# Kernel optimization log

Hardware: AMD Instinct MI355X
Metric: run time of the kernel (lower is better)

## Reference

```python
import jax, jax.numpy as jnp
import numpy as np
from jax import lax

B, N, D = 8, 1024, 768      # batch, tokens, feature dim
H, Y = 12, 64               # heads, head dim
M = 3072                    # hopfield memories (4*D)
STEPS = 12                  # descent steps (module default)
ALPHA = 0.1                 # SGD step size (module default)
BETA = 1.0 / np.sqrt(Y)     # attention inverse temperature
EPS = 1e-5


def setup_inputs() -> dict:
    key = jax.random.key(0)
    k0, k1, k2, k3 = jax.random.split(key, 4)
    return {
        "x": jax.random.normal(k0, (B, N, D), dtype=jnp.float32),
        "ln_gamma": jnp.ones((D,), dtype=jnp.float32),
        "ln_beta": jnp.zeros((D,), dtype=jnp.float32),
        "wq": jax.random.normal(k1, (H, Y, D), dtype=jnp.float32) * 0.02,
        "wk": jax.random.normal(k2, (H, Y, D), dtype=jnp.float32) * 0.02,
        "xi": jax.random.normal(k3, (M, D), dtype=jnp.float32) * 0.02,
    }


def _layer_norm(x, gamma, beta):
    mu = jnp.mean(x, axis=-1, keepdims=True)
    var = jnp.var(x, axis=-1, keepdims=True)
    return gamma * (x - mu) * lax.rsqrt(var + EPS) + beta


def _energy(g, wq, wk, xi):
    # Attention energy: A[b,h,m,n] = sum_y K_{hy m} Q_{hy n}
    q = jnp.einsum("hyd,bnd->bhny", wq, g)
    k = jnp.einsum("hyd,bnd->bhny", wk, g)
    logits = BETA * jnp.einsum("bhmy,bhny->bhmn", k, q)  # [B,H,N(keys),N(queries)]
    e_att = -(1.0 / BETA) * jnp.sum(jax.scipy.special.logsumexp(logits, axis=2))
    # Hopfield energy: -0.5 * sum relu(xi @ g)^2
    hid = jnp.einsum("md,bnd->bnm", xi, g)
    e_hn = -0.5 * jnp.sum(jnp.square(jax.nn.relu(hid)))
    return e_att + e_hn


_energy_grad = jax.grad(_energy)


def reference(x, ln_gamma, ln_beta, wq, wk, xi):
    def step(x, _):
        g = _layer_norm(x, ln_gamma, ln_beta)  # grad taken w.r.t. g, not through LN
        grad = _energy_grad(g, wq, wk, xi)
        return x - ALPHA * grad, None

    x, _ = lax.scan(step, x, None, length=STEPS)
    return x
```

## Files before the change

kernel.cpp:

```cpp
#include <hip/hip_runtime.h>
#include <math.h>

#define B_ 8
#define N_ 1024
#define D_ 768
#define H_ 12
#define Y_ 64
#define M_ 3072
#define STEPS_ 12
#define ALPHA_ 0.1f
#define BETA_ 0.125f
#define EPS_ 1e-5f

typedef __attribute__((ext_vector_type(8))) short bf16x8;
typedef __attribute__((ext_vector_type(8))) unsigned short u16x8;
typedef __attribute__((ext_vector_type(4))) float f32x4;

__device__ inline unsigned short f2bf(float f) {
  union { float f; unsigned int u; } v; v.f = f;
  unsigned int r = (v.u + 0x7fffu + ((v.u >> 16) & 1u)) >> 16;
  return (unsigned short)r;
}

__device__ inline void async_copy16(const void* g, void* l) {
  __builtin_amdgcn_global_load_lds(
      (const __attribute__((address_space(1))) unsigned int*)g,
      (__attribute__((address_space(3))) unsigned int*)l, 16, 0, 0);
}

__device__ inline int xcd_remap(int bid, int nwg) {
  const int qd = nwg >> 3, rm = nwg & 7;
  const int xcd = bid & 7, idx = bid >> 3;
  return (xcd < rm ? xcd * (qd + 1) : rm * (qd + 1) + (xcd - rm) * qd) + idx;
}

__global__ __launch_bounds__(256) void ln_kernel(const float* __restrict__ x,
    const float* __restrict__ gamma, const float* __restrict__ beta,
    unsigned short* __restrict__ g) {
  const int row = blockIdx.x;
  const int t = threadIdx.x;
  const float* xr = x + (size_t)row * D_;
  float v0 = xr[t], v1 = xr[t + 256], v2 = xr[t + 512];
  float s = v0 + v1 + v2;
  float sq = v0 * v0 + v1 * v1 + v2 * v2;
  #pragma unroll
  for (int off = 1; off < 64; off <<= 1) {
    s += __shfl_xor(s, off);
    sq += __shfl_xor(sq, off);
  }
  __shared__ float ss[4], ssq[4];
  const int wid = t >> 6;
  if ((t & 63) == 0) { ss[wid] = s; ssq[wid] = sq; }
  __syncthreads();
  s = ss[0] + ss[1] + ss[2] + ss[3];
  sq = ssq[0] + ssq[1] + ssq[2] + ssq[3];
  const float mu = s * (1.0f / D_);
  const float var = sq * (1.0f / D_) - mu * mu;
  const float r = rsqrtf(var + EPS_);
  unsigned short* gr = g + (size_t)row * D_;
  gr[t]       = f2bf(gamma[t]       * (v0 - mu) * r + beta[t]);
  gr[t + 256] = f2bf(gamma[t + 256] * (v1 - mu) * r + beta[t + 256]);
  gr[t + 512] = f2bf(gamma[t + 512] * (v2 - mu) * r + beta[t + 512]);
}

__global__ __launch_bounds__(256) void cvt_bf16(const float* __restrict__ in,
    unsigned short* __restrict__ out, int n) {
  int i = blockIdx.x * 256 + threadIdx.x;
  if (i < n) out[i] = f2bf(in[i]);
}

__global__ __launch_bounds__(256) void transpose_cvt(const float* __restrict__ in,
    unsigned short* __restrict__ out, int R, int C, int ldo, int koff) {
  __shared__ float tile[32][33];
  const int c0 = blockIdx.x * 32, r0 = blockIdx.y * 32;
  const int tx = threadIdx.x & 31, ty = threadIdx.x >> 5;
  #pragma unroll
  for (int i = 0; i < 32; i += 8)
    tile[ty + i][tx] = in[(size_t)(r0 + ty + i) * C + c0 + tx];
  __syncthreads();
  #pragma unroll
  for (int i = 0; i < 32; i += 8)
    out[(size_t)(c0 + ty + i) * ldo + koff + r0 + tx] = f2bf(tile[tx][ty + i]);
}

template <bool RELU, bool WRT>
__global__ __launch_bounds__(256) void gemm128(
    const unsigned short* __restrict__ A, const unsigned short* __restrict__ Bm,
    unsigned short* __restrict__ C, int N, int K, int gridN,
    unsigned short* __restrict__ qT, unsigned short* __restrict__ kT) {
  __shared__ __align__(16) unsigned short As[128 * 64];
  __shared__ __align__(16) unsigned short Bs[128 * 64];
  const int t = threadIdx.x;
  const int f = xcd_remap(blockIdx.x, gridDim.x);
  const int n0 = (f % gridN) * 128;
  const int m0 = (f / gridN) * 128;
  const int w = t >> 6;
  const int l = t & 63;
  const int wr = (w >> 1) * 64;
  const int wc = (w & 1) * 64;

  f32x4 acc[4][4];
  #pragma unroll
  for (int m = 0; m < 4; ++m)
    #pragma unroll
    for (int n = 0; n < 4; ++n) {
      f32x4 z = {0.f, 0.f, 0.f, 0.f};
      acc[m][n] = z;
    }

  for (int kt = 0; kt < K; kt += 64) {
    #pragma unroll
    for (int i = 0; i < 4; ++i) {
      const int flat = i * 4096 + t * 16;
      const int row = flat >> 7;
      const int slog = ((flat >> 4) & 7) ^ (row & 7);
      async_copy16(A + (size_t)(m0 + row) * K + kt + slog * 8, (char*)As + flat);
      async_copy16(Bm + (size_t)(n0 + row) * K + kt + slog * 8, (char*)Bs + flat);
    }
    __syncthreads();
    #pragma unroll
    for (int kk = 0; kk < 2; ++kk) {
      bf16x8 a[4], b[4];
      const int lr = l & 15;
      const int sl = kk * 4 + (l >> 4);
      #pragma unroll
      for (int m = 0; m < 4; ++m) {
        const int row = wr + m * 16 + lr;
        a[m] = *(const bf16x8*)((const char*)As + row * 128 + ((sl ^ (row & 7)) << 4));
      }
      #pragma unroll
      for (int n = 0; n < 4; ++n) {
        const int row = wc + n * 16 + lr;
        b[n] = *(const bf16x8*)((const char*)Bs + row * 128 + ((sl ^ (row & 7)) << 4));
      }
      #pragma unroll
      for (int m = 0; m < 4; ++m)
        #pragma unroll
        for (int n = 0; n < 4; ++n)
          acc[m][n] = __builtin_amdgcn_mfma_f32_16x16x32_bf16(a[m], b[n], acc[m][n], 0, 0, 0);
    }
    __syncthreads();
  }

  const int cr = (l >> 4) * 4;
  const int cc = l & 15;
  #pragma unroll
  for (int m = 0; m < 4; ++m)
    #pragma unroll
    for (int n = 0; n < 4; ++n) {
      const int col = n0 + wc + n * 16 + cc;
      unsigned long long pk = 0;
      #pragma unroll
      for (int j = 0; j < 4; ++j) {
        const int row = m0 + wr + m * 16 + cr + j;
        float v = acc[m][n][j];
        if (RELU) v = v > 0.f ? v : 0.f;
        const unsigned short bv = f2bf(v);
        C[(size_t)row * N + col] = bv;
        if (WRT) pk |= (unsigned long long)bv << (16 * j);
      }
      if (WRT) {
        const int row0 = m0 + wr + m * 16 + cr;
        const int bb = row0 >> 10, nn = row0 & 1023;
        const int hy = (col < 768) ? col : (col - 768);
        unsigned short* T = (col < 768) ? qT : kT;
        *(unsigned long long*)(T + ((size_t)bb * 768 + hy) * N_ + nn) = pk;
      }
    }
}

__global__ __launch_bounds__(256) void gemm_update(
    const unsigned short* __restrict__ A1,
    const unsigned short* __restrict__ A2,
    const unsigned short* __restrict__ B2,
    float* __restrict__ x,
    float alpha) {
  __shared__ __align__(16) unsigned short As[128 * 64];
  __shared__ __align__(16) unsigned short Bs[64 * 64];
  const int t = threadIdx.x;
  const int f = xcd_remap(blockIdx.x, gridDim.x);
  const int n0 = (f % 12) * 64;
  const int m0 = (f / 12) * 128;
  const int w = t >> 6;
  const int l = t & 63;
  const int wr = (w >> 1) * 64;
  const int wc = (w & 1) * 32;

  f32x4 acc[4][2];
  #pragma unroll
  for (int m = 0; m < 4; ++m)
    #pragma unroll
    for (int n = 0; n < 2; ++n) {
      f32x4 z = {0.f, 0.f, 0.f, 0.f};
      acc[m][n] = z;
    }

  for (int kt = 0; kt < 4608; kt += 64) {
    #pragma unroll
    for (int i = 0; i < 4; ++i) {
      const int flat = i * 4096 + t * 16;
      const int row = flat >> 7;
      const int slog = ((flat >> 4) & 7) ^ (row & 7);
      const unsigned short* src = (kt < 1536)
          ? A1 + (size_t)(m0 + row) * 1536 + kt + slog * 8
          : A2 + (size_t)(m0 + row) * 3072 + (kt - 1536) + slog * 8;
      async_copy16(src, (char*)As + flat);
    }
    #pragma unroll
    for (int i = 0; i < 2; ++i) {
      const int flat = i * 4096 + t * 16;
      const int row = flat >> 7;
      const int slog = ((flat >> 4) & 7) ^ (row & 7);
      async_copy16(B2 + (size_t)(n0 + row) * 4608 + kt + slog * 8, (char*)Bs + flat);
    }
    __syncthreads();
    #pragma unroll
    for (int kk = 0; kk < 2; ++kk) {
      bf16x8 a[4], b[2];
      const int lr = l & 15;
      const int sl = kk * 4 + (l >> 4);
      #pragma unroll
      for (int m = 0; m < 4; ++m) {
        const int row = wr + m * 16 + lr;
        a[m] = *(const bf16x8*)((const char*)As + row * 128 + ((sl ^ (row & 7)) << 4));
      }
      #pragma unroll
      for (int n = 0; n < 2; ++n) {
        const int row = wc + n * 16 + lr;
        b[n] = *(const bf16x8*)((const char*)Bs + row * 128 + ((sl ^ (row & 7)) << 4));
      }
      #pragma unroll
      for (int m = 0; m < 4; ++m)
        #pragma unroll
        for (int n = 0; n < 2; ++n)
          acc[m][n] = __builtin_amdgcn_mfma_f32_16x16x32_bf16(a[m], b[n], acc[m][n], 0, 0, 0);
    }
    __syncthreads();
  }

  const int cr = (l >> 4) * 4;
  const int cc = l & 15;
  #pragma unroll
  for (int m = 0; m < 4; ++m)
    #pragma unroll
    for (int n = 0; n < 2; ++n) {
      const int col = n0 + wc + n * 16 + cc;
      #pragma unroll
      for (int j = 0; j < 4; ++j) {
        const int row = m0 + wr + m * 16 + cr + j;
        float* cp = x + (size_t)row * 768 + col;
        *cp += alpha * acc[m][n][j];
      }
    }
}

__global__ __launch_bounds__(256) void attn1_mfma(
    const unsigned short* __restrict__ qk, const unsigned short* __restrict__ kT,
    unsigned short* __restrict__ AqAk, float* __restrict__ lse) {
  __shared__ __align__(16) unsigned short Ks[128 * 64];
  __shared__ __align__(16) unsigned short KTs[64 * 128];
  __shared__ __align__(16) unsigned short Ps[4 * 16 * 128];
  const int n0 = blockIdx.x * 64;
  const int h = blockIdx.y;
  const int b = blockIdx.z;
  const int t = threadIdx.x;
  const int w = t >> 6;
  const int l = t & 63;
  const int g = l >> 4;
  const int ql = l & 15;
  char* psw = (char*)(Ps + w * 2048);
  const int LD = 1536;

  bf16x8 qf[2];
  {
    const unsigned short* qrow =
        qk + ((size_t)(b * N_ + n0 + w * 16 + ql)) * LD + h * Y_;
    qf[0] = *(const bf16x8*)(qrow + g * 8);
    qf[1] = *(const bf16x8*)(qrow + 32 + g * 8);
  }
  const unsigned short* kbase = qk + (size_t)b * N_ * LD + 768 + h * Y_;
  const unsigned short* kTbase = kT + ((size_t)(b * H_ + h)) * Y_ * N_;

  f32x4 acc[4];
  #pragma unroll
  for (int yf = 0; yf < 4; ++yf) { f32x4 z = {0.f,0.f,0.f,0.f}; acc[yf] = z; }
  float mmax = -1e30f, lsum = 0.f;

  for (int mc = 0; mc < N_; mc += 128) {
    #pragma unroll
    for (int i = 0; i < 4; ++i) {
      const int flat = i * 4096 + t * 16;
      const int row = flat >> 7;
      const int slog = ((flat >> 4) & 7) ^ (row & 7);
      async_copy16(kbase + (size_t)(mc + row) * LD + slog * 8, (char*)Ks + flat);
    }
    #pragma unroll
    for (int i = 0; i < 4; ++i) {
      const int flat = i * 4096 + t * 16;
      const int row = flat >> 8;
      const int slog = ((flat >> 4) & 15) ^ (row & 7);
      async_copy16(kTbase + (size_t)row * N_ + mc + slog * 8, (char*)KTs + flat);
    }
    __syncthreads();

    f32x4 s[8];
    __builtin_amdgcn_s_setprio(1);
    #pragma unroll
    for (int f = 0; f < 8; ++f) {
      f32x4 z = {0.f,0.f,0.f,0.f}; s[f] = z;
      #pragma unroll
      for (int ks = 0; ks < 2; ++ks) {
        const int key = f * 16 + ql;
        bf16x8 a = *(const bf16x8*)((const char*)Ks + key * 128 +
                                    (((ks * 4 + g) ^ (key & 7)) << 4));
        s[f] = __builtin_amdgcn_mfma_f32_16x16x32_bf16(a, qf[ks], s[f], 0, 0, 0);
      }
    }
    __builtin_amdgcn_s_setprio(0);
    float rm = -1e30f;
    #pragma unroll
    for (int f = 0; f < 8; ++f)
      #pragma unroll
      for (int j = 0; j < 4; ++j) {
        const float v = s[f][j] * BETA_;
        s[f][j] = v;
        rm = fmaxf(rm, v);
      }
    rm = fmaxf(rm, __shfl_xor(rm, 16));
    rm = fmaxf(rm, __shfl_xor(rm, 32));
    const float nm = fmaxf(mmax, rm);
    const float sc = __expf(mmax - nm);
    float rs = 0.f;
    #pragma unroll
    for (int f = 0; f < 8; ++f) {
      unsigned short p4[4];
      #pragma unroll
      for (int j = 0; j < 4; ++j) {
        const float pvj = __expf(s[f][j] - nm);
        rs += pvj;
        p4[j] = f2bf(pvj);
      }
      unsigned long long pk = (unsigned long long)p4[0] |
          ((unsigned long long)p4[1] << 16) |
          ((unsigned long long)p4[2] << 32) |
          ((unsigned long long)p4[3] << 48);
      const int sl = (f * 4 + g) ^ ((ql & 7) << 1);
      *(unsigned long long*)(psw + ql * 256 + sl * 8) = pk;
    }
    rs += __shfl_xor(rs, 16);
    rs += __shfl_xor(rs, 32);
    lsum = lsum * sc + rs;
    mmax = nm;
    #pragma unroll
    for (int yf = 0; yf < 4; ++yf) acc[yf] *= sc;
    __builtin_amdgcn_s_setprio(1);
    #pragma unroll
    for (int ks2 = 0; ks2 < 4; ++ks2) {
      const int sl2 = (ks2 * 8 + g * 2) ^ ((ql & 7) << 1);
      bf16x8 pa = *(const bf16x8*)(psw + ql * 256 + sl2 * 8);
      #pragma unroll
      for (int yf = 0; yf < 4; ++yf) {
        const int y = yf * 16 + ql;
        bf16x8 bk = *(const bf16x8*)((const char*)KTs + y * 256 +
                                     (((ks2 * 4 + g) ^ (y & 7)) << 4));
        acc[yf] = __builtin_amdgcn_mfma_f32_16x16x32_bf16(pa, bk, acc[yf], 0, 0, 0);
      }
    }
    __builtin_amdgcn_s_setprio(0);
    __syncthreads();
  }

  float linv[4];
  #pragma unroll
  for (int j = 0; j < 4; ++j)
    linv[j] = 1.0f / __shfl(lsum, (g << 4) + g * 4 + j);
  #pragma unroll
  for (int yf = 0; yf < 4; ++yf)
    #pragma unroll
    for (int j = 0; j < 4; ++j) {
      const int row = n0 + w * 16 + g * 4 + j;
      AqAk[((size_t)(b * N_ + row)) * LD + h * Y_ + yf * 16 + ql] =
          f2bf(acc[yf][j] * linv[j]);
    }
  if (g == 0)
    lse[((size_t)b * H_ + h) * N_ + n0 + w * 16 + ql] = mmax + __logf(lsum);
}

__global__ __launch_bounds__(256) void attn2_mfma(
    const unsigned short* __restrict__ qk, const unsigned short* __restrict__ qT,
    const float* __restrict__ lse, unsigned short* __restrict__ AqAk) {
  __shared__ __align__(16) unsigned short Qs[128 * 64];
  __shared__ __align__(16) unsigned short QTs[64 * 128];
  __shared__ __align__(16) unsigned short Ws[4 * 16 * 128];
  __shared__ float lse_s[128];
  const int m0 = blockIdx.x * 64;
  const int h = blockIdx.y;
  const int b = blockIdx.z;
  const int t = threadIdx.x;
  const int w = t >> 6;
  const int l = t & 63;
  const int g = l >> 4;
  const int ql = l & 15;
  char* wsw = (char*)(Ws + w * 2048);
  const int LD = 1536;

  bf16x8 ka[2];
  {
    const unsigned short* krow =
        qk + ((size_t)(b * N_ + m0 + w * 16 + ql)) * LD + 768 + h * Y_;
    ka[0] = *(const bf16x8*)(krow + g * 8);
    ka[1] = *(const bf16x8*)(krow + 32 + g * 8);
  }
  const unsigned short* qbase = qk + (size_t)b * N_ * LD + h * Y_;
  const unsigned short* qTbase = qT + ((size_t)(b * H_ + h)) * Y_ * N_;
  const float* lbase = lse + ((size_t)b * H_ + h) * N_;

  f32x4 acc[4];
  #pragma unroll
  for (int yf = 0; yf < 4; ++yf) { f32x4 z = {0.f,0.f,0.f,0.f}; acc[yf] = z; }

  for (int nc = 0; nc < N_; nc += 128) {
    #pragma unroll
    for (int i = 0; i < 4; ++i) {
      const int flat = i * 4096 + t * 16;
      const int row = flat >> 7;
      const int slog = ((flat >> 4) & 7) ^ (row & 7);
      async_copy16(qbase + (size_t)(nc + row) * LD + slog * 8, (char*)Qs + flat);
    }
    #pragma unroll
    for (int i = 0; i < 4; ++i) {
      const int flat = i * 4096 + t * 16;
      const int row = flat >> 8;
      const int slog = ((flat >> 4) & 15) ^ (row & 7);
      async_copy16(qTbase + (size_t)row * N_ + nc + slog * 8, (char*)QTs + flat);
    }
    if (t < 128) lse_s[t] = lbase[nc + t];
    __syncthreads();

    f32x4 s[8];
    __builtin_amdgcn_s_setprio(1);
    #pragma unroll
    for (int f = 0; f < 8; ++f) {
      f32x4 z = {0.f,0.f,0.f,0.f}; s[f] = z;
      #pragma unroll
      for (int ks = 0; ks < 2; ++ks) {
        const int qr = f * 16 + ql;
        bf16x8 a = *(const bf16x8*)((const char*)Qs + qr * 128 +
                                    (((ks * 4 + g) ^ (qr & 7)) << 4));
        s[f] = __builtin_amdgcn_mfma_f32_16x16x32_bf16(a, ka[ks], s[f], 0, 0, 0);
      }
    }
    __builtin_amdgcn_s_setprio(0);
    #pragma unroll
    for (int f = 0; f < 8; ++f) {
      unsigned short w4[4];
      #pragma unroll
      for (int j = 0; j < 4; ++j) {
        const float wv = __expf(s[f][j] * BETA_ - lse_s[f * 16 + g * 4 + j]);
        w4[j] = f2bf(wv);
      }
      unsigned long long pk =
          (unsigned long long)w4[0] | ((unsigned long long)w4[1] << 16) |
          ((unsigned long long)w4[2] << 32) | ((unsigned long long)w4[3] << 48);
      const int sl = (f * 4 + g) ^ ((ql & 7) << 1);
      *(unsigned long long*)(wsw + ql * 256 + sl * 8) = pk;
    }
    __builtin_amdgcn_s_setprio(1);
    #pragma unroll
    for (int ks2 = 0; ks2 < 4; ++ks2) {
      const int sl2 = (ks2 * 8 + g * 2) ^ ((ql & 7) << 1);
      bf16x8 wa = *(const bf16x8*)(wsw + ql * 256 + sl2 * 8);
      #pragma unroll
      for (int yf = 0; yf < 4; ++yf) {
        const int y = yf * 16 + ql;
        bf16x8 bq = *(const bf16x8*)((const char*)QTs + y * 256 +
                                     (((ks2 * 4 + g) ^ (y & 7)) << 4));
        acc[yf] = __builtin_amdgcn_mfma_f32_16x16x32_bf16(wa, bq, acc[yf], 0, 0, 0);
      }
    }
    __builtin_amdgcn_s_setprio(0);
    __syncthreads();
  }

  #pragma unroll
  for (int yf = 0; yf < 4; ++yf)
    #pragma unroll
    for (int j = 0; j < 4; ++j) {
      const int row = m0 + w * 16 + g * 4 + j;
      AqAk[((size_t)(b * N_ + row)) * LD + 768 + h * Y_ + yf * 16 + ql] =
          f2bf(acc[yf][j]);
    }
}

extern "C" void kernel_launch(void* const* d_in, const int* in_sizes, int n_in,
                              void* d_out, int out_size, void* d_ws, size_t ws_size,
                              hipStream_t stream) {
  const float* x0    = (const float*)d_in[0];
  const float* gamma = (const float*)d_in[1];
  const float* beta  = (const float*)d_in[2];
  const float* wq    = (const float*)d_in[3];
  const float* wk    = (const float*)d_in[4];
  const float* xi    = (const float*)d_in[5];
  float* x = (float*)d_out;

  const size_t SZ = (size_t)B_ * N_ * D_;
  char* wsp = (char*)d_ws;
  size_t off = 0;
  auto alloc = [&](size_t bytes) -> void* {
    off = (off + 255) & ~(size_t)255;
    void* p = wsp + off;
    off += bytes;
    return p;
  };
  unsigned short* g_bf   = (unsigned short*)alloc(SZ * 2);
  unsigned short* qk_bf  = (unsigned short*)alloc(SZ * 2 * 2);
  unsigned short* AqAk   = (unsigned short*)alloc(SZ * 2 * 2);
  unsigned short* qT_bf  = (unsigned short*)alloc(SZ * 2);
  unsigned short* kT_bf  = (unsigned short*)alloc(SZ * 2);
  float*          lse    = (float*)alloc((size_t)B_ * H_ * N_ * 4);
  unsigned short* wqk_bf = (unsigned short*)alloc((size_t)2 * D_ * D_ * 2);
  unsigned short* xi_bf  = (unsigned short*)alloc((size_t)M_ * D_ * 2);
  unsigned short* B2_bf  = (unsigned short*)alloc((size_t)D_ * (2 * D_ + M_) * 2);
  off = (off + 255) & ~(size_t)255;
  unsigned short* hid_bf = (unsigned short*)(wsp + off);
  size_t avail = ws_size > off ? ws_size - off : 0;
  long rmax = (long)(avail / ((size_t)M_ * 2));
  int R = (int)((rmax / 128) * 128);
  if (R > B_ * N_) R = B_ * N_;
  if (R < 128) R = 128;

  const int WQN = D_ * D_;
  const int XIN = M_ * D_;
  cvt_bf16<<<(WQN + 255) / 256, 256, 0, stream>>>(wq, wqk_bf, WQN);
  cvt_bf16<<<(WQN + 255) / 256, 256, 0, stream>>>(wk, wqk_bf + (size_t)D_ * D_, WQN);
  cvt_bf16<<<(XIN + 255) / 256, 256, 0, stream>>>(xi, xi_bf, XIN);
  const int LDB2 = 2 * D_ + M_;
  transpose_cvt<<<dim3(D_ / 32, D_ / 32), 256, 0, stream>>>(wq, B2_bf, D_, D_, LDB2, 0);
  transpose_cvt<<<dim3(D_ / 32, D_ / 32), 256, 0, stream>>>(wk, B2_bf, D_, D_, LDB2, D_);
  transpose_cvt<<<dim3(D_ / 32, M_ / 32), 256, 0, stream>>>(xi, B2_bf, M_, D_, LDB2, 2 * D_);

  hipMemcpyAsync(x, x0, SZ * sizeof(float), hipMemcpyDeviceToDevice, stream);

  const int MN = B_ * N_;
  for (int step = 0; step < STEPS_; ++step) {
    ln_kernel<<<MN, 256, 0, stream>>>(x, gamma, beta, g_bf);
    gemm128<false, true><<<(1536 / 128) * (MN / 128), 256, 0, stream>>>(
        g_bf, wqk_bf, qk_bf, 1536, D_, 1536 / 128, qT_bf, kT_bf);
    attn1_mfma<<<dim3(N_ / 64, H_, B_), 256, 0, stream>>>(qk_bf, kT_bf, AqAk, lse);
    attn2_mfma<<<dim3(N_ / 64, H_, B_), 256, 0, stream>>>(qk_bf, qT_bf, lse, AqAk);
    for (int r0 = 0; r0 < MN; r0 += R) {
      const int rows = (MN - r0) < R ? (MN - r0) : R;
      gemm128<true, false><<<(M_ / 128) * (rows / 128), 256, 0, stream>>>(
          g_bf + (size_t)r0 * D_, xi_bf, hid_bf, M_, D_, M_ / 128, nullptr, nullptr);
      gemm_update<<<(D_ / 64) * (rows / 128), 256, 0, stream>>>(
          AqAk + (size_t)r0 * 1536, hid_bf, B2_bf, x + (size_t)r0 * D_, ALPHA_);
    }
  }
}
```

Measured before the change: 3.282 ms.

## Fuse QK and Hopfield projection GEMMs and deepen update GEMM K-tile

Merges the QK projection GEMM and the relu(xi·g) hidden GEMM into one launch over a 36-column-tile grid, so the shared LN output is read by a single kernel. The chunked hidden-buffer loop is removed: the full B*N x M hidden buffer is allocated and the update GEMM runs once over all rows. The update GEMM's K tile grows from 64 to 128, with a 16-way swizzle to match, to halve barrier count per K. This needs a larger workspace (about 50 MB for hid) and doubles the update kernel's LDS use, which may reduce occupancy.

```diff
diff --git a/kernel.cpp b/kernel.cpp
--- a/kernel.cpp
+++ b/kernel.cpp
@@ -83,21 +83,24 @@
     out[(size_t)(c0 + ty + i) * ldo + koff + r0 + tx] = f2bf(tile[tx][ty + i]);
 }
 
-template <bool RELU, bool WRT>
-__global__ __launch_bounds__(256) void gemm128(
-    const unsigned short* __restrict__ A, const unsigned short* __restrict__ Bm,
-    unsigned short* __restrict__ C, int N, int K, int gridN,
+__global__ __launch_bounds__(256) void gemm_fused(
+    const unsigned short* __restrict__ A, const unsigned short* __restrict__ Bqk,
+    const unsigned short* __restrict__ Bxi, unsigned short* __restrict__ qk,
+    unsigned short* __restrict__ hid,
     unsigned short* __restrict__ qT, unsigned short* __restrict__ kT) {
   __shared__ __align__(16) unsigned short As[128 * 64];
   __shared__ __align__(16) unsigned short Bs[128 * 64];
   const int t = threadIdx.x;
   const int f = xcd_remap(blockIdx.x, gridDim.x);
-  const int n0 = (f % gridN) * 128;
-  const int m0 = (f / gridN) * 128;
+  const int n0 = (f % 36) * 128;
+  const int m0 = (f / 36) * 128;
   const int w = t >> 6;
   const int l = t & 63;
   const int wr = (w >> 1) * 64;
   const int wc = (w & 1) * 64;
+  const bool isQK = (n0 < 1536);
+  const unsigned short* Bsrc = isQK ? (Bqk + (size_t)n0 * D_)
+                                    : (Bxi + (size_t)(n0 - 1536) * D_);
 
   f32x4 acc[4][4];
   #pragma unroll
@@ -108,14 +111,14 @@
       acc[m][n] = z;
     }
 
-  for (int kt = 0; kt < K; kt += 64) {
+  for (int kt = 0; kt < D_; kt += 64) {
     #pragma unroll
     for (int i = 0; i < 4; ++i) {
       const int flat = i * 4096 + t * 16;
       const int row = flat >> 7;
       const int slog = ((flat >> 4) & 7) ^ (row & 7);
-      async_copy16(A + (size_t)(m0 + row) * K + kt + slog * 8, (char*)As + flat);
-      async_copy16(Bm + (size_t)(n0 + row) * K + kt + slog * 8, (char*)Bs + flat);
+      async_copy16(A + (size_t)(m0 + row) * D_ + kt + slog * 8, (char*)As + flat);
+      async_copy16(Bsrc + (size_t)row * D_ + kt + slog * 8, (char*)Bs + flat);
     }
     __syncthreads();
     #pragma unroll
@@ -149,22 +152,29 @@
     #pragma unroll
     for (int n = 0; n < 4; ++n) {
       const int col = n0 + wc + n * 16 + cc;
-      unsigned long long pk = 0;
-      #pragma unroll
-      for (int j = 0; j < 4; ++j) {
-        const int row = m0 + wr + m * 16 + cr + j;
-        float v = acc[m][n][j];
-        if (RELU) v = v > 0.f ? v : 0.f;
-        const unsigned short bv = f2bf(v);
-        C[(size_t)row * N + col] = bv;
-        if (WRT) pk |= (unsigned long long)bv << (16 * j);
-      }
-      if (WRT) {
+      if (isQK) {
+        unsigned long long pk = 0;
+        #pragma unroll
+        for (int j = 0; j < 4; ++j) {
+          const int row = m0 + wr + m * 16 + cr + j;
+          const unsigned short bv = f2bf(acc[m][n][j]);
+          qk[(size_t)row * 1536 + col] = bv;
+          pk |= (unsigned long long)bv << (16 * j);
+        }
         const int row0 = m0 + wr + m * 16 + cr;
         const int bb = row0 >> 10, nn = row0 & 1023;
         const int hy = (col < 768) ? col : (col - 768);
         unsigned short* T = (col < 768) ? qT : kT;
         *(unsigned long long*)(T + ((size_t)bb * 768 + hy) * N_ + nn) = pk;
+      } else {
+        const int hcol = col - 1536;
+        #pragma unroll
+        for (int j = 0; j < 4; ++j) {
+          const int row = m0 + wr + m * 16 + cr + j;
+          float v = acc[m][n][j];
+          v = v > 0.f ? v : 0.f;
+          hid[(size_t)row * 3072 + hcol] = f2bf(v);
+        }
       }
     }
 }
@@ -175,8 +185,8 @@
     const unsigned short* __restrict__ B2,
     float* __restrict__ x,
     float alpha) {
-  __shared__ __align__(16) unsigned short As[128 * 64];
-  __shared__ __align__(16) unsigned short Bs[64 * 64];
+  __shared__ __align__(16) unsigned short As[128 * 128];
+  __shared__ __align__(16) unsigned short Bs[64 * 128];
   const int t = threadIdx.x;
   const int f = xcd_remap(blockIdx.x, gridDim.x);
   const int n0 = (f % 12) * 64;
@@ -195,39 +205,39 @@
       acc[m][n] = z;
     }
 
-  for (int kt = 0; kt < 4608; kt += 64) {
-    #pragma unroll
-    for (int i = 0; i < 4; ++i) {
-      const int flat = i * 4096 + t * 16;
-      const int row = flat >> 7;
-      const int slog = ((flat >> 4) & 7) ^ (row & 7);
+  for (int kt = 0; kt < 4608; kt += 128) {
+    #pragma unroll
+    for (int i = 0; i < 8; ++i) {
+      const int flat = i * 4096 + t * 16;
+      const int row = flat >> 8;
+      const int slog = ((flat >> 4) & 15) ^ (row & 15);
       const unsigned short* src = (kt < 1536)
           ? A1 + (size_t)(m0 + row) * 1536 + kt + slog * 8
           : A2 + (size_t)(m0 + row) * 3072 + (kt - 1536) + slog * 8;
       async_copy16(src, (char*)As + flat);
     }
     #pragma unroll
-    for (int i = 0; i < 2; ++i) {
-      const int flat = i * 4096 + t * 16;
-      const int row = flat >> 7;
-      const int slog = ((flat >> 4) & 7) ^ (row & 7);
+    for (int i = 0; i < 4; ++i) {
+      const int flat = i * 4096 + t * 16;
+      const int row = flat >> 8;
+      const int slog = ((flat >> 4) & 15) ^ (row & 15);
       async_copy16(B2 + (size_t)(n0 + row) * 4608 + kt + slog * 8, (char*)Bs + flat);
     }
     __syncthreads();
     #pragma unroll
-    for (int kk = 0; kk < 2; ++kk) {
+    for (int kk = 0; kk < 4; ++kk) {
       bf16x8 a[4], b[2];
       const int lr = l & 15;
       const int sl = kk * 4 + (l >> 4);
       #pragma unroll
       for (int m = 0; m < 4; ++m) {
         const int row = wr + m * 16 + lr;
-        a[m] = *(const bf16x8*)((const char*)As + row * 128 + ((sl ^ (row & 7)) << 4));
+        a[m] = *(const bf16x8*)((const char*)As + row * 256 + ((sl ^ (row & 15)) << 4));
       }
       #pragma unroll
       for (int n = 0; n < 2; ++n) {
         const int row = wc + n * 16 + lr;
-        b[n] = *(const bf16x8*)((const char*)Bs + row * 128 + ((sl ^ (row & 7)) << 4));
+        b[n] = *(const bf16x8*)((const char*)Bs + row * 256 + ((sl ^ (row & 15)) << 4));
       }
       #pragma unroll
       for (int m = 0; m < 4; ++m)
@@ -521,13 +531,7 @@
   unsigned short* wqk_bf = (unsigned short*)alloc((size_t)2 * D_ * D_ * 2);
   unsigned short* xi_bf  = (unsigned short*)alloc((size_t)M_ * D_ * 2);
   unsigned short* B2_bf  = (unsigned short*)alloc((size_t)D_ * (2 * D_ + M_) * 2);
-  off = (off + 255) & ~(size_t)255;
-  unsigned short* hid_bf = (unsigned short*)(wsp + off);
-  size_t avail = ws_size > off ? ws_size - off : 0;
-  long rmax = (long)(avail / ((size_t)M_ * 2));
-  int R = (int)((rmax / 128) * 128);
-  if (R > B_ * N_) R = B_ * N_;
-  if (R < 128) R = 128;
+  unsigned short* hid_bf = (unsigned short*)alloc((size_t)B_ * N_ * M_ * 2);
 
   const int WQN = D_ * D_;
   const int XIN = M_ * D_;
@@ -544,16 +548,11 @@
   const int MN = B_ * N_;
   for (int step = 0; step < STEPS_; ++step) {
     ln_kernel<<<MN, 256, 0, stream>>>(x, gamma, beta, g_bf);
-    gemm128<false, true><<<(1536 / 128) * (MN / 128), 256, 0, stream>>>(
-        g_bf, wqk_bf, qk_bf, 1536, D_, 1536 / 128, qT_bf, kT_bf);
+    gemm_fused<<<36 * (MN / 128), 256, 0, stream>>>(
+        g_bf, wqk_bf, xi_bf, qk_bf, hid_bf, qT_bf, kT_bf);
     attn1_mfma<<<dim3(N_ / 64, H_, B_), 256, 0, stream>>>(qk_bf, kT_bf, AqAk, lse);
     attn2_mfma<<<dim3(N_ / 64, H_, B_), 256, 0, stream>>>(qk_bf, qT_bf, lse, AqAk);
-    for (int r0 = 0; r0 < MN; r0 += R) {
-      const int rows = (MN - r0) < R ? (MN - r0) : R;
-      gemm128<true, false><<<(M_ / 128) * (rows / 128), 256, 0, stream>>>(
-          g_bf + (size_t)r0 * D_, xi_bf, hid_bf, M_, D_, M_ / 128, nullptr, nullptr);
-      gemm_update<<<(D_ / 64) * (rows / 128), 256, 0, stream>>>(
-          AqAk + (size_t)r0 * 1536, hid_bf, B2_bf, x + (size_t)r0 * D_, ALPHA_);
-    }
-  }
-}
+    gemm_update<<<12 * (MN / 128), 256, 0, stream>>>(
+        AqAk, hid_bf, B2_bf, x, ALPHA_);
+  }
+}
```

New measurement: 3.428 ms. 1.04x slower.
